# Kernel tuning notes

Measured on AMD Instinct MI355X. Metric: run time of the kernel, lower is better.

The kernel has to match this reference:

```python
import jax, jax.numpy as jnp
import numpy as np

D = 1024
H = 16
HD = D // H          # 64
D2 = D // 2          # 512
B = 2
N = 1024


def setup_inputs() -> dict:
    key = jax.random.key(0)
    ks = jax.random.split(key, 12)
    std = 0.02
    init_std = 0.02 / np.sqrt(D)  # matches _init_weights for value/output proj
    return {
        "h": jax.random.normal(ks[0], (B, N, D), jnp.float32),
        "prev_idx": jax.random.randint(ks[1], (B, N), 0, N),
        # forward encoders: Linear(d, d/2) -> GELU -> Linear(d/2, 1), stacked over heads
        "fw_W1": jax.random.normal(ks[2], (H, D2, D), jnp.float32) * std,
        "fw_b1": jnp.zeros((H, D2), jnp.float32),
        "fw_W2": jax.random.normal(ks[3], (H, D2), jnp.float32) * std,  # out-dim 1 squeezed
        "fw_b2": jnp.zeros((H,), jnp.float32),
        # backward encoders
        "bw_W1": jax.random.normal(ks[4], (H, D2, D), jnp.float32) * std,
        "bw_b1": jnp.zeros((H, D2), jnp.float32),
        "bw_W2": jax.random.normal(ks[5], (H, D2), jnp.float32) * std,
        "bw_b2": jnp.zeros((H,), jnp.float32),
        # per-head value projection Linear(d, head_dim, bias=False)
        "Wv": jax.random.normal(ks[6], (H, HD, D), jnp.float32) * init_std,
        # relation fusion: Linear(3*hd, hd) -> GELU -> Linear(hd, hd)
        "fu_W1": jax.random.normal(ks[7], (H, HD, 3 * HD), jnp.float32) * std,
        "fu_b1": jnp.zeros((H, HD), jnp.float32),
        "fu_W2": jax.random.normal(ks[8], (H, HD, HD), jnp.float32) * std,
        "fu_b2": jnp.zeros((H, HD), jnp.float32),
        # output projection Linear(d, d, bias=False)
        "Wo": jax.random.normal(ks[9], (D, D), jnp.float32) * init_std,
        "chain_ratio": jnp.float32(0.5),
    }


def _encoder_logits(h, W1, b1, W2, b2):
    # h: [B,N,D]; W1: [H,D2,D]; returns [H,B,N]
    x = jnp.einsum('bnd,hkd->hbnk', h, W1) + b1[:, None, None, :]
    x = jax.nn.gelu(x, approximate=False)  # torch nn.GELU default = exact erf
    return jnp.einsum('hbnk,hk->hbn', x, W2) + b2[:, None, None]


def reference(h, prev_idx, fw_W1, fw_b1, fw_W2, fw_b2,
              bw_W1, bw_b1, bw_W2, bw_b2,
              Wv, fu_W1, fu_b1, fu_W2, fu_b2, Wo, chain_ratio):
    pos = jnp.arange(N, dtype=h.dtype)

    fwd_logits = _encoder_logits(h, fw_W1, fw_b1, fw_W2, fw_b2)  # [H,B,N]
    bwd_logits = _encoder_logits(h, bw_W1, bw_b1, bw_W2, bw_b2)  # [H,B,N]

    # faithful to original: softmax over an N-wise expansion of a scalar logit
    fwd_probs = jax.nn.softmax(
        jnp.broadcast_to(fwd_logits[..., None], (H, B, N, N)), axis=-1)
    bwd_probs = jax.nn.softmax(
        jnp.broadcast_to(bwd_logits[..., None], (H, B, N, N)), axis=-1)

    fwd_targets = jnp.sum(fwd_probs * pos, axis=-1).astype(jnp.int32)  # [H,B,N]
    bwd_targets = jnp.sum(bwd_probs * pos, axis=-1).astype(jnp.int32)

    # chaining with prev_idx (prev_idx is given)
    chain_threshold = jnp.floor(jax.nn.sigmoid(chain_ratio) * N)
    should_chain = jnp.arange(N) >= chain_threshold  # [N]
    prev_clamped = jnp.clip(prev_idx, 0, N - 1).astype(jnp.int32)  # [B,N]
    fwd_targets = jnp.where(should_chain[None, None, :],
                            prev_clamped[None, :, :], fwd_targets)

    head_features = jnp.einsum('bnd,hed->hbne', h, Wv)  # [H,B,N,HD]
    fwd_feats = jnp.einsum('hbnm,hbme->hbne', fwd_probs, head_features)
    bwd_feats = jnp.einsum('hbnm,hbme->hbne', bwd_probs, head_features)

    rel = jnp.concatenate([head_features, fwd_feats, bwd_feats], axis=-1)  # [H,B,N,3HD]
    x = jax.nn.gelu(jnp.einsum('hbnc,hec->hbne', rel, fu_W1)
                    + fu_b1[:, None, None, :], approximate=False)
    head_out = jnp.einsum('hbne,hfe->hbnf', x, fu_W2) + fu_b2[:, None, None, :]

    multi = jnp.transpose(head_out, (1, 2, 0, 3)).reshape(B, N, D)
    final_output = jnp.einsum('bnd,ed->bne', multi, Wo)

    eps = 1e-8
    fwd_strength = 1.0 - jnp.sum(fwd_probs * jnp.log(fwd_probs + eps), axis=-1)
    bwd_strength = 1.0 - jnp.sum(bwd_probs * jnp.log(bwd_probs + eps), axis=-1)
    avg_strength = jnp.mean((fwd_strength + bwd_strength) * 0.5, axis=0)  # [B,N]

    return (final_output, fwd_targets[0], bwd_targets[0], avg_strength)
```

## Files before the change

kernel.cpp:

```cpp
#include <hip/hip_runtime.h>
#include <hip/hip_bf16.h>


typedef __attribute__((ext_vector_type(8))) short bf16x8;
typedef __attribute__((ext_vector_type(4))) float f32x4;

#define OFF_HBF  0
#define OFF_XBF  1048576
#define OFF_WVBF 2097152
#define OFF_MBF  2621440
#define OFF_W1A  3145728
#define OFF_HBAR 3178496
#define OFF_BIAS 3180544
#define OFF_C    3181568

__device__ __forceinline__ unsigned short f2bf(float f) {
    unsigned int u = __float_as_uint(f);
    u += 0x7fffu + ((u >> 16) & 1u);
    return (unsigned short)(u >> 16);
}

__device__ __forceinline__ void async_load16(const void* g, void* l) {
    __builtin_amdgcn_global_load_lds(
        (const __attribute__((address_space(1))) unsigned int*)g,
        (__attribute__((address_space(3))) unsigned int*)l, 16, 0, 0);
}

__global__ __launch_bounds__(256) void k_prep1(const float* __restrict__ h,
                                               const float* __restrict__ Wv,
                                               const float* __restrict__ fu_W1,
                                               unsigned short* __restrict__ hbf,
                                               unsigned short* __restrict__ Wvbf,
                                               unsigned short* __restrict__ W1abf,
                                               float* __restrict__ hbar) {
    int blk = blockIdx.x, tid = threadIdx.x;
    if (blk < 128) {
        int b = blk >> 6, chunk = blk & 63;
        int n0 = chunk * 16, d0 = tid * 4;
        const float* hb = h + (size_t)b * 1048576 + d0;
        unsigned short* ob = hbf + (size_t)b * 1048576 + d0;
        float4 sum = make_float4(0.f, 0.f, 0.f, 0.f);
#pragma unroll
        for (int i = 0; i < 16; ++i) {
            float4 v = *(const float4*)(hb + (size_t)(n0 + i) * 1024);
            sum.x += v.x; sum.y += v.y; sum.z += v.z; sum.w += v.w;
            *(ushort4*)(ob + (size_t)(n0 + i) * 1024) =
                make_ushort4(f2bf(v.x), f2bf(v.y), f2bf(v.z), f2bf(v.w));
        }
        float* hp = hbar + b * 1024 + d0;
        atomicAdd(hp + 0, sum.x * (1.f / 1024.f));
        atomicAdd(hp + 1, sum.y * (1.f / 1024.f));
        atomicAdd(hp + 2, sum.z * (1.f / 1024.f));
        atomicAdd(hp + 3, sum.w * (1.f / 1024.f));
    } else if (blk < 1152) {
        int i0 = (blk - 128) * 1024 + tid * 4;
        float4 v = *(const float4*)(Wv + i0);
        *(ushort4*)(Wvbf + i0) =
            make_ushort4(f2bf(v.x), f2bf(v.y), f2bf(v.z), f2bf(v.w));
    } else {
        int blk2 = blk - 1152;
        int hh = blk2 >> 2, q = blk2 & 3;
        int e = q * 16 + (tid >> 4);
        int k4 = (tid & 15) * 4;
        float4 v = *(const float4*)(fu_W1 + (size_t)(hh * 64 + e) * 192 + k4);
        *(ushort4*)(W1abf + hh * 4096 + e * 64 + k4) =
            make_ushort4(f2bf(v.x), f2bf(v.y), f2bf(v.z), f2bf(v.w));
    }
}

__global__ __launch_bounds__(256) void k_prep2(const float* __restrict__ Wo,
                                               const float* __restrict__ fu_W2,
                                               const float* __restrict__ fu_b2,
                                               const float* __restrict__ Wv,
                                               const float* __restrict__ fu_W1,
                                               const float* __restrict__ fu_b1,
                                               const float* __restrict__ hbar,
                                               unsigned short* __restrict__ Mbf,
                                               float* __restrict__ bias,
                                               float* __restrict__ cvec) {
    __shared__ float smem[8384];
    int blk = blockIdx.x, tid = threadIdx.x;
    if (blk < 256) {
        float* W2s = smem;
        float* Wos = smem + 4160;
        float* b2s = smem + 8320;
        int rc = blk >> 4, hh = blk & 15;
        int r0 = rc * 64;
#pragma unroll
        for (int i = 0; i < 16; ++i) {
            int idx = tid + i * 256;
            int f = idx >> 6, e = idx & 63;
            W2s[f * 65 + e] = fu_W2[hh * 4096 + idx];
            Wos[f * 65 + e] = Wo[(size_t)(r0 + f) * 1024 + hh * 64 + e];
        }
        if (tid < 64) b2s[tid] = fu_b2[hh * 64 + tid];
        __syncthreads();
        int ty = tid >> 3, tx = tid & 7;
        int r1 = 2 * ty, r2 = 2 * ty + 1, e0 = tx * 8;
        float acc0[8], acc1[8];
#pragma unroll
        for (int j = 0; j < 8; ++j) { acc0[j] = 0.f; acc1[j] = 0.f; }
        for (int f = 0; f < 64; ++f) {
            float a0 = Wos[r1 * 65 + f], a1 = Wos[r2 * 65 + f];
            const float* w2r = &W2s[f * 65 + e0];
#pragma unroll
            for (int j = 0; j < 8; ++j) {
                float b = w2r[j];
                acc0[j] += a0 * b;
                acc1[j] += a1 * b;
            }
        }
        unsigned short* m1 = Mbf + (size_t)(r0 + r1) * 1024 + hh * 64 + e0;
        unsigned short* m2 = Mbf + (size_t)(r0 + r2) * 1024 + hh * 64 + e0;
        *(ushort4*)(m1) = make_ushort4(f2bf(acc0[0]), f2bf(acc0[1]), f2bf(acc0[2]), f2bf(acc0[3]));
        *(ushort4*)(m1 + 4) = make_ushort4(f2bf(acc0[4]), f2bf(acc0[5]), f2bf(acc0[6]), f2bf(acc0[7]));
        *(ushort4*)(m2) = make_ushort4(f2bf(acc1[0]), f2bf(acc1[1]), f2bf(acc1[2]), f2bf(acc1[3]));
        *(ushort4*)(m2 + 4) = make_ushort4(f2bf(acc1[4]), f2bf(acc1[5]), f2bf(acc1[6]), f2bf(acc1[7]));
        if (tid < 64) {
            float p = 0.f;
#pragma unroll 8
            for (int f = 0; f < 64; ++f) p += Wos[tid * 65 + f] * b2s[f];
            atomicAdd(&bias[r0 + tid], p);
        }
    } else {
        float* psum = smem;
        float* mf = smem + 256;
        int blk2 = blk - 256;
        int b = blk2 >> 4, hh = blk2 & 15;
        int e = tid >> 2, sl = tid & 3;
        const float* wrow = Wv + (size_t)(hh * 64 + e) * 1024;
        const float* hb = hbar + b * 1024;
        float s = 0.f;
        int k0 = sl * 256;
        for (int k = k0; k < k0 + 256; ++k) s += wrow[k] * hb[k];
        psum[e * 4 + sl] = s;
        __syncthreads();
        if (tid < 64)
            mf[tid] = psum[tid * 4] + psum[tid * 4 + 1] + psum[tid * 4 + 2] + psum[tid * 4 + 3];
        __syncthreads();
        if (tid < 64) {
            const float* w1 = fu_W1 + (size_t)(hh * 64 + tid) * 192;
            float acc = fu_b1[hh * 64 + tid];
            for (int k = 0; k < 64; ++k) acc += (w1[64 + k] + w1[128 + k]) * mf[k];
            cvec[b * 1024 + hh * 64 + tid] = acc;
        }
    }
}

template <int MODE>
__global__ __launch_bounds__(256) void k_mm(const unsigned short* __restrict__ A,
                                            const unsigned short* __restrict__ Bw,
                                            void* __restrict__ CoutV,
                                            const unsigned short* __restrict__ W1a,
                                            const float* __restrict__ cvec,
                                            const float* __restrict__ bias,
                                            const int* __restrict__ prev_idx,
                                            const float* __restrict__ chain_ratio) {
    __shared__ __align__(16) char smem[24576];
    const int tid = threadIdx.x;
    const int w = tid >> 6, lane = tid & 63;
    const int rowBase = blockIdx.x * 32, colBase = blockIdx.y * 64;
    const int wmh = (w >> 1) * 16, wnh = (w & 1) * 32;
    const int lr = lane >> 3;
    const int ssrc = ((lane & 7) ^ lr) * 8;
    const int m_lane = lane & 15, quad = lane >> 4;

    if (MODE == 0 && blockIdx.x == 0 && blockIdx.y == 0) {
        float* out = (float*)CoutV;
        float cr = chain_ratio[0];
        float thr = floorf(1024.0f / (1.0f + expf(-cr)));
        float strength = 1.0f - logf(1.0f / 1024.0f + 1e-8f);
        for (int i = tid; i < 2048; i += 256) {
            int n = i & 1023;
            float fwd = 511.0f;
            if ((float)n >= thr) {
                int p = prev_idx[i];
                p = p < 0 ? 0 : (p > 1023 ? 1023 : p);
                fwd = (float)p;
            }
            out[2097152 + i] = fwd;
            out[2097152 + 2048 + i] = 511.0f;
            out[2097152 + 4096 + i] = strength;
        }
    }

    const unsigned short* Ag = A + (size_t)(rowBase + w * 8 + lr) * 1024 + ssrc;
    const unsigned short* Bg0 = Bw + (size_t)(colBase + w * 8 + lr) * 1024 + ssrc;
    const unsigned short* Bg1 = Bg0 + (size_t)32 * 1024;
    const int woff = w * 1024;

    f32x4 acc[2];
    acc[0] = (f32x4){0.f, 0.f, 0.f, 0.f};
    acc[1] = (f32x4){0.f, 0.f, 0.f, 0.f};

    async_load16(Ag, smem + woff);
    async_load16(Bg0, smem + 8192 + woff);
    async_load16(Bg1, smem + 8192 + woff + 4096);

    for (int k0 = 0; k0 < 1024; k0 += 64) {
        const int cur = (k0 >> 6) & 1;
        char* Asc = smem + cur * 4096;
        char* Bsc = smem + 8192 + cur * 8192;
        __syncthreads();
        if (k0 + 64 < 1024) {
            char* Asn = smem + (cur ^ 1) * 4096;
            char* Bsn = smem + 8192 + (cur ^ 1) * 8192;
            async_load16(Ag + k0 + 64, Asn + woff);
            async_load16(Bg0 + k0 + 64, Bsn + woff);
            async_load16(Bg1 + k0 + 64, Bsn + woff + 4096);
        }
#pragma unroll
        for (int kh = 0; kh < 2; ++kh) {
            const int seg = kh * 4 + quad;
            const int m = wmh + m_lane;
            bf16x8 af = *(const bf16x8*)(Asc + m * 128 + ((seg ^ (m & 7)) << 4));
#pragma unroll
            for (int nt = 0; nt < 2; ++nt) {
                int n = wnh + nt * 16 + m_lane;
                bf16x8 bfr = *(const bf16x8*)(Bsc + n * 128 + ((seg ^ (n & 7)) << 4));
                acc[nt] = __builtin_amdgcn_mfma_f32_16x16x32_bf16(af, bfr, acc[nt], 0, 0, 0);
            }
        }
    }

    char* As = smem;
    char* Bs = smem + 8192;
    if (MODE == 0) {
        float* out = (float*)CoutV;
        float* Os = (float*)smem;
        __syncthreads();
#pragma unroll
        for (int nt = 0; nt < 2; ++nt) {
            int c = wnh + nt * 16 + m_lane;
            float bj = bias[colBase + c];
#pragma unroll
            for (int r4 = 0; r4 < 4; ++r4) {
                int r = wmh + quad * 4 + r4;
                Os[r * 68 + c] = acc[nt][r4] + bj;
            }
        }
        __syncthreads();
#pragma unroll
        for (int j = 0; j < 2; ++j) {
            int sidx = tid + j * 256;
            int r = sidx >> 4, sc = sidx & 15;
            float4 v = *(const float4*)&Os[r * 68 + sc * 4];
            *(float4*)&out[(size_t)(rowBase + r) * 1024 + colBase + sc * 4] = v;
        }
    } else {
        unsigned short* Xbf = (unsigned short*)CoutV;
        const int hh = blockIdx.y;
        __syncthreads();
        const unsigned short* Wg = W1a + hh * 4096 + (w * 8 + lr) * 64 + ssrc;
        async_load16(Wg, Bs + woff);
        async_load16(Wg + 32 * 64, Bs + woff + 4096);
#pragma unroll
        for (int nt = 0; nt < 2; ++nt) {
            int c = wnh + nt * 16 + m_lane;
#pragma unroll
            for (int r4 = 0; r4 < 4; ++r4) {
                int r = wmh + quad * 4 + r4;
                *(unsigned short*)(As + r * 128 + (((c >> 3) ^ (r & 7)) << 4) +
                                   (c & 7) * 2) = f2bf(acc[nt][r4]);
            }
        }
        __syncthreads();
        f32x4 acc2[2];
        acc2[0] = (f32x4){0.f, 0.f, 0.f, 0.f};
        acc2[1] = (f32x4){0.f, 0.f, 0.f, 0.f};
#pragma unroll
        for (int kh = 0; kh < 2; ++kh) {
            const int seg = kh * 4 + quad;
            const int m = wmh + m_lane;
            bf16x8 af = *(const bf16x8*)(As + m * 128 + ((seg ^ (m & 7)) << 4));
#pragma unroll
            for (int nt = 0; nt < 2; ++nt) {
                int n = wnh + nt * 16 + m_lane;
                bf16x8 bfr = *(const bf16x8*)(Bs + n * 128 + ((seg ^ (n & 7)) << 4));
                acc2[nt] = __builtin_amdgcn_mfma_f32_16x16x32_bf16(af, bfr, acc2[nt], 0, 0, 0);
            }
        }
        __syncthreads();
        const int b = rowBase >> 10;
#pragma unroll
        for (int nt = 0; nt < 2; ++nt) {
            int c = wnh + nt * 16 + m_lane;
            float cadd = cvec[b * 1024 + hh * 64 + c];
#pragma unroll
            for (int r4 = 0; r4 < 4; ++r4) {
                int r = wmh + quad * 4 + r4;
                float t = acc2[nt][r4] + cadd;
                t = 0.5f * t * (1.0f + erff(t * 0.70710678118654752f));
                *(unsigned short*)(As + r * 128 + c * 2) = f2bf(t);
            }
        }
        __syncthreads();
        int r = tid >> 3, s = tid & 7;
        float4 v = *(const float4*)(As + r * 128 + s * 16);
        *(float4*)((char*)Xbf + ((size_t)(rowBase + r) * 1024 + colBase + s * 8) * 2) = v;
    }
}

extern "C" void kernel_launch(void* const* d_in, const int* in_sizes, int n_in,
                              void* d_out, int out_size, void* d_ws, size_t ws_size,
                              hipStream_t stream) {
    const float* h      = (const float*)d_in[0];
    const int*   prev   = (const int*)d_in[1];
    const float* Wv     = (const float*)d_in[10];
    const float* fu_W1  = (const float*)d_in[11];
    const float* fu_b1  = (const float*)d_in[12];
    const float* fu_W2  = (const float*)d_in[13];
    const float* fu_b2  = (const float*)d_in[14];
    const float* Wo     = (const float*)d_in[15];
    const float* cratio = (const float*)d_in[16];

    float* out = (float*)d_out;
    float* ws  = (float*)d_ws;
    unsigned short* hbf   = (unsigned short*)(ws + OFF_HBF);
    unsigned short* Xbf   = (unsigned short*)(ws + OFF_XBF);
    unsigned short* Wvbf  = (unsigned short*)(ws + OFF_WVBF);
    unsigned short* Mbf   = (unsigned short*)(ws + OFF_MBF);
    unsigned short* W1abf = (unsigned short*)(ws + OFF_W1A);
    float* hbar = ws + OFF_HBAR;
    float* bias = ws + OFF_BIAS;
    float* cv   = ws + OFF_C;

    hipMemsetAsync(hbar, 0, 3072 * sizeof(float), stream);
    k_prep1<<<1216, 256, 0, stream>>>(h, Wv, fu_W1, hbf, Wvbf, W1abf, hbar);
    k_prep2<<<288, 256, 0, stream>>>(Wo, fu_W2, fu_b2, Wv, fu_W1, fu_b1, hbar,
                                     Mbf, bias, cv);
    k_mm<1><<<dim3(64, 16), 256, 0, stream>>>(hbf, Wvbf, Xbf, W1abf, cv,
                                              nullptr, nullptr, nullptr);
    k_mm<0><<<dim3(64, 16), 256, 0, stream>>>(Xbf, Mbf, out, nullptr, nullptr,
                                              bias, prev, cratio);
}
```

Baseline: 176.5 us.

## Fold fusion W1a into value projection weights to drop second per-head GEMM

Precomputes G = fu_W1[:, :, :64] @ Wv per head in the prep kernel, so the first main GEMM multiplies h directly by the combined weight and applies bias plus GELU without a second in-block MFMA stage. This removes the per-tile W1a load, the bf16 staging of the intermediate and the extra 64x64 MFMA pass in k_mm<1>. In exchange the prep kernel does a small FP32 matrix product per head (scalar loop reading fu_W1 from global), and the folded weights are rounded to bf16 once rather than the intermediate, which slightly changes numerics.

```diff
diff --git a/kernel.cpp b/kernel.cpp
--- a/kernel.cpp
+++ b/kernel.cpp
@@ -7,9 +7,8 @@
 
 #define OFF_HBF  0
 #define OFF_XBF  1048576
-#define OFF_WVBF 2097152
+#define OFF_GBF  2097152
 #define OFF_MBF  2621440
-#define OFF_W1A  3145728
 #define OFF_HBAR 3178496
 #define OFF_BIAS 3180544
 #define OFF_C    3181568
@@ -30,9 +29,9 @@
                                                const float* __restrict__ Wv,
                                                const float* __restrict__ fu_W1,
                                                unsigned short* __restrict__ hbf,
-                                               unsigned short* __restrict__ Wvbf,
-                                               unsigned short* __restrict__ W1abf,
+                                               unsigned short* __restrict__ Gbf,
                                                float* __restrict__ hbar) {
+    __shared__ float smem[4160];
     int blk = blockIdx.x, tid = threadIdx.x;
     if (blk < 128) {
         int b = blk >> 6, chunk = blk & 63;
@@ -52,19 +51,43 @@
         atomicAdd(hp + 1, sum.y * (1.f / 1024.f));
         atomicAdd(hp + 2, sum.z * (1.f / 1024.f));
         atomicAdd(hp + 3, sum.w * (1.f / 1024.f));
-    } else if (blk < 1152) {
-        int i0 = (blk - 128) * 1024 + tid * 4;
-        float4 v = *(const float4*)(Wv + i0);
-        *(ushort4*)(Wvbf + i0) =
-            make_ushort4(f2bf(v.x), f2bf(v.y), f2bf(v.z), f2bf(v.w));
     } else {
-        int blk2 = blk - 1152;
-        int hh = blk2 >> 2, q = blk2 & 3;
-        int e = q * 16 + (tid >> 4);
-        int k4 = (tid & 15) * 4;
-        float4 v = *(const float4*)(fu_W1 + (size_t)(hh * 64 + e) * 192 + k4);
-        *(ushort4*)(W1abf + hh * 4096 + e * 64 + k4) =
-            make_ushort4(f2bf(v.x), f2bf(v.y), f2bf(v.z), f2bf(v.w));
+        int g = blk - 128;
+        int hh = g >> 3, q = g & 7;
+        int c0 = q * 128;
+        int cl = tid & 63;
+        int ebu = __builtin_amdgcn_readfirstlane(tid >> 6) * 16;
+        const float* w1base = fu_W1 + (size_t)(hh * 64) * 192;
+#pragma unroll
+        for (int sc = 0; sc < 2; ++sc) {
+            if (sc) __syncthreads();
+#pragma unroll
+            for (int i = 0; i < 16; ++i) {
+                int idx = tid + i * 256;
+                int r = idx >> 6, cc = idx & 63;
+                smem[r * 65 + cc] =
+                    Wv[(size_t)(hh * 64 + r) * 1024 + c0 + sc * 64 + cc];
+            }
+            __syncthreads();
+            float acc[16];
+#pragma unroll
+            for (int e = 0; e < 16; ++e) acc[e] = 0.f;
+            for (int ep = 0; ep < 64; ep += 4) {
+                float wv0 = smem[(ep + 0) * 65 + cl];
+                float wv1 = smem[(ep + 1) * 65 + cl];
+                float wv2 = smem[(ep + 2) * 65 + cl];
+                float wv3 = smem[(ep + 3) * 65 + cl];
+#pragma unroll
+                for (int e = 0; e < 16; ++e) {
+                    const float* w1 = w1base + (size_t)(ebu + e) * 192 + ep;
+                    acc[e] += w1[0] * wv0 + w1[1] * wv1 + w1[2] * wv2 + w1[3] * wv3;
+                }
+            }
+            unsigned short* gp =
+                Gbf + (size_t)(hh * 64 + ebu) * 1024 + c0 + sc * 64 + cl;
+#pragma unroll
+            for (int e = 0; e < 16; ++e) gp[(size_t)e * 1024] = f2bf(acc[e]);
+        }
     }
 }
 
@@ -151,7 +174,6 @@
 __global__ __launch_bounds__(256) void k_mm(const unsigned short* __restrict__ A,
                                             const unsigned short* __restrict__ Bw,
                                             void* __restrict__ CoutV,
-                                            const unsigned short* __restrict__ W1a,
                                             const float* __restrict__ cvec,
                                             const float* __restrict__ bias,
                                             const int* __restrict__ prev_idx,
@@ -224,7 +246,6 @@
     }
 
     char* As = smem;
-    char* Bs = smem + 8192;
     if (MODE == 0) {
         float* out = (float*)CoutV;
         float* Os = (float*)smem;
@@ -250,38 +271,8 @@
     } else {
         unsigned short* Xbf = (unsigned short*)CoutV;
         const int hh = blockIdx.y;
-        __syncthreads();
-        const unsigned short* Wg = W1a + hh * 4096 + (w * 8 + lr) * 64 + ssrc;
-        async_load16(Wg, Bs + woff);
-        async_load16(Wg + 32 * 64, Bs + woff + 4096);
-#pragma unroll
-        for (int nt = 0; nt < 2; ++nt) {
-            int c = wnh + nt * 16 + m_lane;
-#pragma unroll
-            for (int r4 = 0; r4 < 4; ++r4) {
-                int r = wmh + quad * 4 + r4;
-                *(unsigned short*)(As + r * 128 + (((c >> 3) ^ (r & 7)) << 4) +
-                                   (c & 7) * 2) = f2bf(acc[nt][r4]);
-            }
-        }
-        __syncthreads();
-        f32x4 acc2[2];
-        acc2[0] = (f32x4){0.f, 0.f, 0.f, 0.f};
-        acc2[1] = (f32x4){0.f, 0.f, 0.f, 0.f};
-#pragma unroll
-        for (int kh = 0; kh < 2; ++kh) {
-            const int seg = kh * 4 + quad;
-            const int m = wmh + m_lane;
-            bf16x8 af = *(const bf16x8*)(As + m * 128 + ((seg ^ (m & 7)) << 4));
-#pragma unroll
-            for (int nt = 0; nt < 2; ++nt) {
-                int n = wnh + nt * 16 + m_lane;
-                bf16x8 bfr = *(const bf16x8*)(Bs + n * 128 + ((seg ^ (n & 7)) << 4));
-                acc2[nt] = __builtin_amdgcn_mfma_f32_16x16x32_bf16(af, bfr, acc2[nt], 0, 0, 0);
-            }
-        }
-        __syncthreads();
         const int b = rowBase >> 10;
+        __syncthreads();
 #pragma unroll
         for (int nt = 0; nt < 2; ++nt) {
             int c = wnh + nt * 16 + m_lane;
@@ -289,14 +280,15 @@
 #pragma unroll
             for (int r4 = 0; r4 < 4; ++r4) {
                 int r = wmh + quad * 4 + r4;
-                float t = acc2[nt][r4] + cadd;
+                float t = acc[nt][r4] + cadd;
                 t = 0.5f * t * (1.0f + erff(t * 0.70710678118654752f));
-                *(unsigned short*)(As + r * 128 + c * 2) = f2bf(t);
+                *(unsigned short*)(As + r * 128 + (((c >> 3) ^ (r & 7)) << 4) +
+                                   (c & 7) * 2) = f2bf(t);
             }
         }
         __syncthreads();
         int r = tid >> 3, s = tid & 7;
-        float4 v = *(const float4*)(As + r * 128 + s * 16);
+        float4 v = *(const float4*)(As + r * 128 + (((s) ^ (r & 7)) << 4));
         *(float4*)((char*)Xbf + ((size_t)(rowBase + r) * 1024 + colBase + s * 8) * 2) = v;
     }
 }
@@ -316,21 +308,20 @@
 
     float* out = (float*)d_out;
     float* ws  = (float*)d_ws;
-    unsigned short* hbf   = (unsigned short*)(ws + OFF_HBF);
-    unsigned short* Xbf   = (unsigned short*)(ws + OFF_XBF);
-    unsigned short* Wvbf  = (unsigned short*)(ws + OFF_WVBF);
-    unsigned short* Mbf   = (unsigned short*)(ws + OFF_MBF);
-    unsigned short* W1abf = (unsigned short*)(ws + OFF_W1A);
+    unsigned short* hbf = (unsigned short*)(ws + OFF_HBF);
+    unsigned short* Xbf = (unsigned short*)(ws + OFF_XBF);
+    unsigned short* Gbf = (unsigned short*)(ws + OFF_GBF);
+    unsigned short* Mbf = (unsigned short*)(ws + OFF_MBF);
     float* hbar = ws + OFF_HBAR;
     float* bias = ws + OFF_BIAS;
     float* cv   = ws + OFF_C;
 
     hipMemsetAsync(hbar, 0, 3072 * sizeof(float), stream);
-    k_prep1<<<1216, 256, 0, stream>>>(h, Wv, fu_W1, hbf, Wvbf, W1abf, hbar);
+    k_prep1<<<256, 256, 0, stream>>>(h, Wv, fu_W1, hbf, Gbf, hbar);
     k_prep2<<<288, 256, 0, stream>>>(Wo, fu_W2, fu_b2, Wv, fu_W1, fu_b1, hbar,
                                      Mbf, bias, cv);
-    k_mm<1><<<dim3(64, 16), 256, 0, stream>>>(hbf, Wvbf, Xbf, W1abf, cv,
+    k_mm<1><<<dim3(64, 16), 256, 0, stream>>>(hbf, Gbf, Xbf, cv,
                                               nullptr, nullptr, nullptr);
-    k_mm<0><<<dim3(64, 16), 256, 0, stream>>>(Xbf, Mbf, out, nullptr, nullptr,
+    k_mm<0><<<dim3(64, 16), 256, 0, stream>>>(Xbf, Mbf, out, nullptr,
                                               bias, prev, cratio);
 }
```

Result: slower. 186.2 us (+5.5%).
